# Kernel tuning notes

Hardware: AMD Instinct MI355X
Metric: run time of the kernel (lower is better)

Reference implementation:

```python
import jax, jax.numpy as jnp
import numpy as np

D_MODEL, D_K, D_V = 512, 64, 64
LN_EPS = 1e-6


def setup_inputs() -> dict:
    key = jax.random.key(0)
    ks = jax.random.split(key, 8)
    B, Lq, Lk = 2, 1024, 1024
    q = jax.random.normal(ks[0], (B, Lq, D_MODEL), dtype=jnp.float32)
    k = jax.random.normal(ks[1], (B, Lk, D_MODEL), dtype=jnp.float32)
    v = jax.random.normal(ks[2], (B, Lk, D_MODEL), dtype=jnp.float32)
    s = 1.0 / np.sqrt(D_MODEL)
    Wq = jax.random.normal(ks[3], (D_MODEL, D_K), dtype=jnp.float32) * s
    Wk = jax.random.normal(ks[4], (D_MODEL, D_K), dtype=jnp.float32) * s
    Wv = jax.random.normal(ks[5], (D_MODEL, D_V), dtype=jnp.float32) * s
    v_param = jax.random.normal(ks[6], (D_K,), dtype=jnp.float32)
    Wfc = jax.random.normal(ks[7], (D_V, D_MODEL), dtype=jnp.float32) / np.sqrt(D_V)
    ln_gamma = jnp.ones((D_MODEL,), dtype=jnp.float32)
    ln_beta = jnp.zeros((D_MODEL,), dtype=jnp.float32)
    return {"q": q, "k": k, "v": v, "Wq": Wq, "Wk": Wk, "Wv": Wv,
            "v_param": v_param, "Wfc": Wfc, "ln_gamma": ln_gamma, "ln_beta": ln_beta}


def reference(q, k, v, Wq, Wk, Wv, v_param, Wfc, ln_gamma, ln_beta):
    residual = q
    qp = q @ Wq                      # [B, Lq, d_k]
    kp = k @ Wk                      # [B, Lk, d_k]
    vp = v @ Wv                      # [B, Lk, d_v]
    # additive (Bahdanau) scores: tanh(q_i + k_j) . v_param  -> [B, Lq, Lk]
    scores = jnp.einsum("bqkd,d->bqk", jnp.tanh(qp[:, :, None, :] + kp[:, None, :, :]), v_param)
    attn = jax.nn.softmax(scores, axis=-1)   # dropout is identity in eval mode
    out = jnp.einsum("bqk,bkv->bqv", attn, vp)
    out = out @ Wfc + residual               # [B, Lq, d_model]
    mu = jnp.mean(out, axis=-1, keepdims=True)
    var = jnp.var(out, axis=-1, keepdims=True)
    out = (out - mu) * jax.lax.rsqrt(var + LN_EPS) * ln_gamma + ln_beta
    return out, attn
```

## Files before the change

kernel.cpp:

```cpp
#include <hip/hip_runtime.h>
#include <cstddef>
#include <cstdint>

#define D_MODEL 512
#define DK 64
#define LQ 1024
#define LK 1024
#define NB 2
#define LN_EPS 1e-6f
#define L2E2 2.8853900817779268f

__device__ __forceinline__ uint32_t pack_bf2(float a, float b) {
  uint32_t ua = __float_as_uint(a), ub = __float_as_uint(b);
  ua = (ua + 0x7fffu + ((ua >> 16) & 1u)) >> 16;
  ub = (ub + 0x7fffu + ((ub >> 16) & 1u)) >> 16;
  return (ub << 16) | ua;
}

#define PR_ROWS 32
__global__ __launch_bounds__(512) void proj_kernel(
    const float* __restrict__ q, const float* __restrict__ k,
    const float* __restrict__ v, const float* __restrict__ Wq,
    const float* __restrict__ Wk, const float* __restrict__ Wv,
    const float* __restrict__ v_param, float2* __restrict__ ab_g,
    uint32_t* __restrict__ ekT, float* __restrict__ vp) {
  __shared__ float rows[PR_ROWS][D_MODEL];
  const int tid = threadIdx.x;
  const int type = blockIdx.x >> 6;
  const int r0 = (blockIdx.x & 63) * PR_ROWS;
  const float* __restrict__ in = (type == 0) ? q : (type == 1) ? k : v;
  const float* __restrict__ W = (type == 0) ? Wq : (type == 1) ? Wk : Wv;
  {
    const float4* __restrict__ in4 = (const float4*)(in + (size_t)r0 * D_MODEL);
    float4* r4 = (float4*)&rows[0][0];
#pragma unroll
    for (int t = 0; t < 8; ++t) r4[tid + 512 * t] = in4[tid + 512 * t];
  }
  __syncthreads();
  const int lane = tid & 63;
  const int wv = tid >> 6;
  const int rglob = r0 + wv * 4;
  const float* __restrict__ Wl = W + lane;
  float c0[4] = {0.f, 0.f, 0.f, 0.f}, c1[4] = {0.f, 0.f, 0.f, 0.f};
#pragma unroll 2
  for (int e = 0; e < D_MODEL; e += 4) {
    float w0 = Wl[(size_t)(e + 0) * DK];
    float w1 = Wl[(size_t)(e + 1) * DK];
    float w2 = Wl[(size_t)(e + 2) * DK];
    float w3 = Wl[(size_t)(e + 3) * DK];
#pragma unroll
    for (int r = 0; r < 4; ++r) {
      float4 x = *(const float4*)&rows[wv * 4 + r][e];
      c0[r] = fmaf(x.x, w0, c0[r]);
      c1[r] = fmaf(x.y, w1, c1[r]);
      c0[r] = fmaf(x.z, w2, c0[r]);
      c1[r] = fmaf(x.w, w3, c1[r]);
    }
  }
  float acc[4];
#pragma unroll
  for (int r = 0; r < 4; ++r) acc[r] = c0[r] + c1[r];
  if (type == 0) {
    float vpar = v_param[lane];
#pragma unroll
    for (int r = 0; r < 4; ++r) {
      float iv = __builtin_amdgcn_exp2f(-L2E2 * acc[r]);
      ab_g[(size_t)(rglob + r) * DK + lane] = make_float2(vpar * iv, iv);
    }
  } else if (type == 1) {
    float e4[4], h4[4];
#pragma unroll
    for (int r = 0; r < 4; ++r) {
      e4[r] = __builtin_amdgcn_exp2f(L2E2 * acc[r]);
      h4[r] = __shfl_down(e4[r], 32);
    }
    if (lane < 32) {
      int b = rglob >> 10, j0 = rglob & 1023;
      uint4 pk;
      pk.x = pack_bf2(e4[0], h4[0]);
      pk.y = pack_bf2(e4[1], h4[1]);
      pk.z = pack_bf2(e4[2], h4[2]);
      pk.w = pack_bf2(e4[3], h4[3]);
      *(uint4*)&ekT[(size_t)b * 32 * LK + (size_t)lane * LK + j0] = pk;
    }
  } else {
#pragma unroll
    for (int r = 0; r < 4; ++r)
      vp[(size_t)(rglob + r) * DK + lane] = acc[r];
  }
}

#define RB 8
__global__ __launch_bounds__(1024, 4) void attn_kernel(
    const float2* __restrict__ ab_g, const uint32_t* __restrict__ ekT,
    const float* __restrict__ vp, const float* __restrict__ resid,
    const float* __restrict__ Wfc, const float* __restrict__ gamma,
    const float* __restrict__ beta, float* __restrict__ out,
    float* __restrict__ attn_out) {
  __shared__ float sc[RB][LK];
  __shared__ float4 ab4s[RB][32];
  __shared__ float4 pvred[16][RB][16];
  __shared__ __align__(16) float ovlT[DK][RB];
  __shared__ float mred[RB][2], sred[RB][2];
  __shared__ float red[2][RB][8];
  const int tid = threadIdx.x;
  const int row0 = blockIdx.x * RB;
  const int batch = row0 >> 10;
  const uint32_t* __restrict__ ekT_b = ekT + (size_t)batch * 32 * LK;
  const float* __restrict__ vp_b = vp + (size_t)batch * LK * DK;

  if (tid < RB * 64) {
    int r = tid >> 6, d = tid & 63;
    float2 abv = ab_g[(size_t)(row0 + r) * DK + d];
    ((float2*)&ab4s[r][d & 31])[d >> 5] = abv;
  }
  __syncthreads();

  {
    const int j = tid;
    float acc[RB];
#pragma unroll
    for (int r = 0; r < RB; ++r) acc[r] = 0.f;
#pragma unroll 4
    for (int dp = 0; dp < 32; ++dp) {
      uint32_t kw = ekT_b[(size_t)dp * LK + j];
      float klo = __uint_as_float(kw << 16);
      float khi = __uint_as_float(kw & 0xffff0000u);
#pragma unroll
      for (int r = 0; r < RB; ++r) {
        float4 ab = ab4s[r][dp];
        float x1 = klo + ab.y, x2 = khi + ab.w;
        float num = fmaf(ab.z, x1, ab.x * x2);
        acc[r] = fmaf(num, __builtin_amdgcn_rcpf(x1 * x2), acc[r]);
      }
    }
#pragma unroll
    for (int r = 0; r < RB; ++r) sc[r][j] = acc[r];
  }
  __syncthreads();

  const int wave = __builtin_amdgcn_readfirstlane(tid >> 6);
  const int lane = tid & 63;

  {
    const int row = wave >> 1, half = wave & 1;
    const int jb = half * 512;
    float m = 1e30f;
#pragma unroll
    for (int i = 0; i < 8; ++i) m = fminf(m, sc[row][jb + i * 64 + lane]);
#pragma unroll
    for (int off = 32; off > 0; off >>= 1) m = fminf(m, __shfl_xor(m, off));
    if (lane == 0) mred[row][half] = m;
    __syncthreads();
    m = fminf(mred[row][0], mred[row][1]);
    float p[8];
    float ssum = 0.f;
#pragma unroll
    for (int i = 0; i < 8; ++i) {
      float e = __builtin_amdgcn_exp2f((m - sc[row][jb + i * 64 + lane]) * L2E2);
      p[i] = e;
      ssum += e;
    }
#pragma unroll
    for (int off = 32; off > 0; off >>= 1) ssum += __shfl_xor(ssum, off);
    if (lane == 0) sred[row][half] = ssum;
    __syncthreads();
    float inv = __builtin_amdgcn_rcpf(sred[row][0] + sred[row][1]);
    float* __restrict__ arow = attn_out + (size_t)(row0 + row) * LK;
#pragma unroll
    for (int i = 0; i < 8; ++i) {
      float pn = p[i] * inv;
      sc[row][jb + i * 64 + lane] = pn;
      arow[jb + i * 64 + lane] = pn;
    }
  }
  __syncthreads();

  {
    const int jj = lane >> 4, l16 = lane & 15;
    const float4* __restrict__ vp4 = (const float4*)vp_b;
    float4 a[RB];
#pragma unroll
    for (int r = 0; r < RB; ++r) a[r] = make_float4(0.f, 0.f, 0.f, 0.f);
#pragma unroll 2
    for (int it = 0; it < 16; ++it) {
      int j = (wave << 6) + (it << 2) + jj;
      float4 vv = vp4[(size_t)j * (DK / 4) + l16];
#pragma unroll
      for (int r = 0; r < RB; ++r) {
        float pw = sc[r][j];
        a[r].x = fmaf(pw, vv.x, a[r].x);
        a[r].y = fmaf(pw, vv.y, a[r].y);
        a[r].z = fmaf(pw, vv.z, a[r].z);
        a[r].w = fmaf(pw, vv.w, a[r].w);
      }
    }
#pragma unroll
    for (int r = 0; r < RB; ++r) {
      a[r].x += __shfl_xor(a[r].x, 16); a[r].y += __shfl_xor(a[r].y, 16);
      a[r].z += __shfl_xor(a[r].z, 16); a[r].w += __shfl_xor(a[r].w, 16);
      a[r].x += __shfl_xor(a[r].x, 32); a[r].y += __shfl_xor(a[r].y, 32);
      a[r].z += __shfl_xor(a[r].z, 32); a[r].w += __shfl_xor(a[r].w, 32);
    }
    if (jj == 0) {
#pragma unroll
      for (int r = 0; r < RB; ++r) pvred[wave][r][l16] = a[r];
    }
  }
  __syncthreads();
  if (tid < 128) {
    int r = tid >> 4, l16 = tid & 15;
    float4 s = make_float4(0.f, 0.f, 0.f, 0.f);
#pragma unroll
    for (int w = 0; w < 16; ++w) {
      float4 t = pvred[w][r][l16];
      s.x += t.x; s.y += t.y; s.z += t.z; s.w += t.w;
    }
    ovlT[l16 * 4 + 0][r] = s.x;
    ovlT[l16 * 4 + 1][r] = s.y;
    ovlT[l16 * 4 + 2][r] = s.z;
    ovlT[l16 * 4 + 3][r] = s.w;
  }
  __syncthreads();

  {
    const int g = tid >> 9, c = tid & 511, rbase = g * 4;
    const int wv8 = (tid >> 6) & 7;
    float y[4];
#pragma unroll
    for (int rr = 0; rr < 4; ++rr)
      y[rr] = resid[(size_t)(row0 + rbase + rr) * D_MODEL + c];
#pragma unroll 4
    for (int e = 0; e < DK; ++e) {
      float w = Wfc[(size_t)e * D_MODEL + c];
      float4 ov = *(const float4*)&ovlT[e][rbase];
      y[0] = fmaf(ov.x, w, y[0]);
      y[1] = fmaf(ov.y, w, y[1]);
      y[2] = fmaf(ov.z, w, y[2]);
      y[3] = fmaf(ov.w, w, y[3]);
    }
#pragma unroll
    for (int rr = 0; rr < 4; ++rr) {
      float s = y[rr];
#pragma unroll
      for (int off = 32; off > 0; off >>= 1) s += __shfl_xor(s, off);
      if (lane == 0) red[0][rbase + rr][wv8] = s;
    }
    __syncthreads();
    float mu[4];
#pragma unroll
    for (int rr = 0; rr < 4; ++rr) {
      float s = 0.f;
#pragma unroll
      for (int w = 0; w < 8; ++w) s += red[0][rbase + rr][w];
      mu[rr] = s * (1.0f / D_MODEL);
    }
#pragma unroll
    for (int rr = 0; rr < 4; ++rr) {
      float d = y[rr] - mu[rr];
      float s = d * d;
#pragma unroll
      for (int off = 32; off > 0; off >>= 1) s += __shfl_xor(s, off);
      if (lane == 0) red[1][rbase + rr][wv8] = s;
    }
    __syncthreads();
    float gg = gamma[c], bb = beta[c];
#pragma unroll
    for (int rr = 0; rr < 4; ++rr) {
      float s = 0.f;
#pragma unroll
      for (int w = 0; w < 8; ++w) s += red[1][rbase + rr][w];
      float var = s * (1.0f / D_MODEL);
      float rstd = rsqrtf(var + LN_EPS);
      out[(size_t)(row0 + rbase + rr) * D_MODEL + c] =
          (y[rr] - mu[rr]) * rstd * gg + bb;
    }
  }
}

extern "C" void kernel_launch(void* const* d_in, const int* in_sizes, int n_in,
                              void* d_out, int out_size, void* d_ws,
                              size_t ws_size, hipStream_t stream) {
  const float* q = (const float*)d_in[0];
  const float* k = (const float*)d_in[1];
  const float* v = (const float*)d_in[2];
  const float* Wq = (const float*)d_in[3];
  const float* Wk = (const float*)d_in[4];
  const float* Wv = (const float*)d_in[5];
  const float* v_param = (const float*)d_in[6];
  const float* Wfc = (const float*)d_in[7];
  const float* gamma = (const float*)d_in[8];
  const float* beta = (const float*)d_in[9];

  float* out = (float*)d_out;
  float* attn = out + (size_t)NB * LQ * D_MODEL;

  float* base = (float*)d_ws;
  float2* ab_g = (float2*)base;
  uint32_t* ekT = (uint32_t*)(base + (size_t)2 * NB * LQ * DK);
  float* vp = base + (size_t)2 * NB * LQ * DK + NB * 32 * LK;

  hipLaunchKernelGGL(proj_kernel, dim3(3 * 64), dim3(512), 0, stream, q, k, v,
                     Wq, Wk, Wv, v_param, ab_g, ekT, vp);
  hipLaunchKernelGGL(attn_kernel, dim3(NB * LQ / RB), dim3(1024), 0, stream,
                     ab_g, ekT, vp, q, Wfc, gamma, beta, out, attn);
}
```

Measured before the change: 64.92 us.

## Split attention kernel into score/softmax and PV+FC+LayerNorm kernels with smaller blocks

Splits the fused 1024-thread attention kernel into two 256-thread kernels. The first computes scores and softmax in registers, four rows by four columns per thread, and writes attn. The second reloads attn from global memory to do the PV product, the FC projection and LayerNorm. The projection kernel also drops to 16 rows per 256-thread block, doubling its grid. The goal is higher occupancy and better latency hiding through smaller blocks. The cost is an extra launch and an extra global round trip of the attention matrix.

```diff
diff --git a/kernel.cpp b/kernel.cpp
--- a/kernel.cpp
+++ b/kernel.cpp
@@ -17,8 +17,8 @@
   return (ub << 16) | ua;
 }
 
-#define PR_ROWS 32
-__global__ __launch_bounds__(512) void proj_kernel(
+#define PR_ROWS 16
+__global__ __launch_bounds__(256, 4) void proj_kernel(
     const float* __restrict__ q, const float* __restrict__ k,
     const float* __restrict__ v, const float* __restrict__ Wq,
     const float* __restrict__ Wk, const float* __restrict__ Wv,
@@ -26,15 +26,15 @@
     uint32_t* __restrict__ ekT, float* __restrict__ vp) {
   __shared__ float rows[PR_ROWS][D_MODEL];
   const int tid = threadIdx.x;
-  const int type = blockIdx.x >> 6;
-  const int r0 = (blockIdx.x & 63) * PR_ROWS;
+  const int type = blockIdx.x >> 7;
+  const int r0 = (blockIdx.x & 127) * PR_ROWS;
   const float* __restrict__ in = (type == 0) ? q : (type == 1) ? k : v;
   const float* __restrict__ W = (type == 0) ? Wq : (type == 1) ? Wk : Wv;
   {
     const float4* __restrict__ in4 = (const float4*)(in + (size_t)r0 * D_MODEL);
     float4* r4 = (float4*)&rows[0][0];
 #pragma unroll
-    for (int t = 0; t < 8; ++t) r4[tid + 512 * t] = in4[tid + 512 * t];
+    for (int t = 0; t < 8; ++t) r4[tid + 256 * t] = in4[tid + 256 * t];
   }
   __syncthreads();
   const int lane = tid & 63;
@@ -85,96 +85,121 @@
     }
   } else {
 #pragma unroll
-    for (int r = 0; r < 4; ++r)
-      vp[(size_t)(rglob + r) * DK + lane] = acc[r];
-  }
-}
-
-#define RB 8
-__global__ __launch_bounds__(1024, 4) void attn_kernel(
+    for (int r = 0; r < 4; ++r) vp[(size_t)(rglob + r) * DK + lane] = acc[r];
+  }
+}
+
+#define RB 4
+__global__ __launch_bounds__(256, 6) void score_kernel(
     const float2* __restrict__ ab_g, const uint32_t* __restrict__ ekT,
-    const float* __restrict__ vp, const float* __restrict__ resid,
-    const float* __restrict__ Wfc, const float* __restrict__ gamma,
-    const float* __restrict__ beta, float* __restrict__ out,
     float* __restrict__ attn_out) {
-  __shared__ float sc[RB][LK];
   __shared__ float4 ab4s[RB][32];
-  __shared__ float4 pvred[16][RB][16];
-  __shared__ __align__(16) float ovlT[DK][RB];
-  __shared__ float mred[RB][2], sred[RB][2];
-  __shared__ float red[2][RB][8];
+  __shared__ float mred[RB][4], sred[RB][4];
   const int tid = threadIdx.x;
   const int row0 = blockIdx.x * RB;
   const int batch = row0 >> 10;
   const uint32_t* __restrict__ ekT_b = ekT + (size_t)batch * 32 * LK;
-  const float* __restrict__ vp_b = vp + (size_t)batch * LK * DK;
-
-  if (tid < RB * 64) {
+  {
     int r = tid >> 6, d = tid & 63;
     float2 abv = ab_g[(size_t)(row0 + r) * DK + d];
     ((float2*)&ab4s[r][d & 31])[d >> 5] = abv;
   }
   __syncthreads();
 
-  {
-    const int j = tid;
-    float acc[RB];
-#pragma unroll
-    for (int r = 0; r < RB; ++r) acc[r] = 0.f;
-#pragma unroll 4
-    for (int dp = 0; dp < 32; ++dp) {
-      uint32_t kw = ekT_b[(size_t)dp * LK + j];
-      float klo = __uint_as_float(kw << 16);
-      float khi = __uint_as_float(kw & 0xffff0000u);
-#pragma unroll
-      for (int r = 0; r < RB; ++r) {
-        float4 ab = ab4s[r][dp];
-        float x1 = klo + ab.y, x2 = khi + ab.w;
+  float acc[RB][4];
+#pragma unroll
+  for (int r = 0; r < RB; ++r)
+#pragma unroll
+    for (int jj = 0; jj < 4; ++jj) acc[r][jj] = 0.f;
+
+#pragma unroll 2
+  for (int dp = 0; dp < 32; ++dp) {
+    float klo[4], khi[4];
+#pragma unroll
+    for (int jj = 0; jj < 4; ++jj) {
+      uint32_t kw = ekT_b[(size_t)dp * LK + tid + jj * 256];
+      klo[jj] = __uint_as_float(kw << 16);
+      khi[jj] = __uint_as_float(kw & 0xffff0000u);
+    }
+#pragma unroll
+    for (int r = 0; r < RB; ++r) {
+      float4 ab = ab4s[r][dp];
+#pragma unroll
+      for (int jj = 0; jj < 4; ++jj) {
+        float x1 = klo[jj] + ab.y, x2 = khi[jj] + ab.w;
         float num = fmaf(ab.z, x1, ab.x * x2);
-        acc[r] = fmaf(num, __builtin_amdgcn_rcpf(x1 * x2), acc[r]);
+        acc[r][jj] = fmaf(num, __builtin_amdgcn_rcpf(x1 * x2), acc[r][jj]);
       }
     }
-#pragma unroll
-    for (int r = 0; r < RB; ++r) sc[r][j] = acc[r];
-  }
-  __syncthreads();
+  }
 
   const int wave = __builtin_amdgcn_readfirstlane(tid >> 6);
   const int lane = tid & 63;
 
   {
-    const int row = wave >> 1, half = wave & 1;
-    const int jb = half * 512;
-    float m = 1e30f;
-#pragma unroll
-    for (int i = 0; i < 8; ++i) m = fminf(m, sc[row][jb + i * 64 + lane]);
-#pragma unroll
-    for (int off = 32; off > 0; off >>= 1) m = fminf(m, __shfl_xor(m, off));
-    if (lane == 0) mred[row][half] = m;
+#pragma unroll
+    for (int r = 0; r < RB; ++r) {
+      float pm = fminf(fminf(acc[r][0], acc[r][1]), fminf(acc[r][2], acc[r][3]));
+#pragma unroll
+      for (int off = 32; off > 0; off >>= 1) pm = fminf(pm, __shfl_xor(pm, off));
+      if (lane == 0) mred[r][wave] = pm;
+    }
     __syncthreads();
-    m = fminf(mred[row][0], mred[row][1]);
-    float p[8];
-    float ssum = 0.f;
-#pragma unroll
-    for (int i = 0; i < 8; ++i) {
-      float e = __builtin_amdgcn_exp2f((m - sc[row][jb + i * 64 + lane]) * L2E2);
-      p[i] = e;
-      ssum += e;
-    }
-#pragma unroll
-    for (int off = 32; off > 0; off >>= 1) ssum += __shfl_xor(ssum, off);
-    if (lane == 0) sred[row][half] = ssum;
+    float inv[RB];
+#pragma unroll
+    for (int r = 0; r < RB; ++r) {
+      float m = fminf(fminf(mred[r][0], mred[r][1]),
+                      fminf(mred[r][2], mred[r][3]));
+      float s = 0.f;
+#pragma unroll
+      for (int jj = 0; jj < 4; ++jj) {
+        float e = __builtin_amdgcn_exp2f((m - acc[r][jj]) * L2E2);
+        acc[r][jj] = e;
+        s += e;
+      }
+#pragma unroll
+      for (int off = 32; off > 0; off >>= 1) s += __shfl_xor(s, off);
+      if (lane == 0) sred[r][wave] = s;
+    }
     __syncthreads();
-    float inv = __builtin_amdgcn_rcpf(sred[row][0] + sred[row][1]);
-    float* __restrict__ arow = attn_out + (size_t)(row0 + row) * LK;
-#pragma unroll
-    for (int i = 0; i < 8; ++i) {
-      float pn = p[i] * inv;
-      sc[row][jb + i * 64 + lane] = pn;
-      arow[jb + i * 64 + lane] = pn;
-    }
-  }
-  __syncthreads();
+#pragma unroll
+    for (int r = 0; r < RB; ++r)
+      inv[r] = __builtin_amdgcn_rcpf(sred[r][0] + sred[r][1] + sred[r][2] +
+                                     sred[r][3]);
+#pragma unroll
+    for (int r = 0; r < RB; ++r) {
+      float* __restrict__ arow = attn_out + (size_t)(row0 + r) * LK;
+#pragma unroll
+      for (int jj = 0; jj < 4; ++jj)
+        arow[tid + jj * 256] = acc[r][jj] * inv[r];
+    }
+  }
+}
+
+__global__ __launch_bounds__(256, 4) void pvfc_kernel(
+    const float* __restrict__ attn, const float* __restrict__ vp,
+    const float* __restrict__ resid, const float* __restrict__ Wfc,
+    const float* __restrict__ gamma, const float* __restrict__ beta,
+    float* __restrict__ out) {
+  __shared__ float sc[RB][LK];
+  __shared__ float4 pvred[4][RB][16];
+  __shared__ __align__(16) float ovlT[DK][RB];
+  __shared__ float red[2][RB][4];
+  const int tid = threadIdx.x;
+  const int row0 = blockIdx.x * RB;
+  const int batch = row0 >> 10;
+  const float* __restrict__ vp_b = vp + (size_t)batch * LK * DK;
+  {
+    const float4* __restrict__ a4 =
+        (const float4*)(attn + (size_t)row0 * LK);
+    float4* s4 = (float4*)&sc[0][0];
+#pragma unroll
+    for (int t = 0; t < 4; ++t) s4[tid + 256 * t] = a4[tid + 256 * t];
+  }
+  __syncthreads();
+
+  const int wave = __builtin_amdgcn_readfirstlane(tid >> 6);
+  const int lane = tid & 63;
 
   {
     const int jj = lane >> 4, l16 = lane & 15;
@@ -182,9 +207,9 @@
     float4 a[RB];
 #pragma unroll
     for (int r = 0; r < RB; ++r) a[r] = make_float4(0.f, 0.f, 0.f, 0.f);
-#pragma unroll 2
-    for (int it = 0; it < 16; ++it) {
-      int j = (wave << 6) + (it << 2) + jj;
+#pragma unroll 4
+    for (int it = 0; it < 64; ++it) {
+      int j = (wave << 8) + (it << 2) + jj;
       float4 vv = vp4[(size_t)j * (DK / 4) + l16];
 #pragma unroll
       for (int r = 0; r < RB; ++r) {
@@ -208,11 +233,11 @@
     }
   }
   __syncthreads();
-  if (tid < 128) {
+  if (tid < 64) {
     int r = tid >> 4, l16 = tid & 15;
     float4 s = make_float4(0.f, 0.f, 0.f, 0.f);
 #pragma unroll
-    for (int w = 0; w < 16; ++w) {
+    for (int w = 0; w < 4; ++w) {
       float4 t = pvred[w][r][l16];
       s.x += t.x; s.y += t.y; s.z += t.z; s.w += t.w;
     }
@@ -224,56 +249,53 @@
   __syncthreads();
 
   {
-    const int g = tid >> 9, c = tid & 511, rbase = g * 4;
-    const int wv8 = (tid >> 6) & 7;
-    float y[4];
-#pragma unroll
-    for (int rr = 0; rr < 4; ++rr)
-      y[rr] = resid[(size_t)(row0 + rbase + rr) * D_MODEL + c];
+    const int c0 = tid, c1 = tid + 256;
+    float y[RB][2];
+#pragma unroll
+    for (int r = 0; r < RB; ++r) {
+      y[r][0] = resid[(size_t)(row0 + r) * D_MODEL + c0];
+      y[r][1] = resid[(size_t)(row0 + r) * D_MODEL + c1];
+    }
 #pragma unroll 4
     for (int e = 0; e < DK; ++e) {
-      float w = Wfc[(size_t)e * D_MODEL + c];
-      float4 ov = *(const float4*)&ovlT[e][rbase];
-      y[0] = fmaf(ov.x, w, y[0]);
-      y[1] = fmaf(ov.y, w, y[1]);
-      y[2] = fmaf(ov.z, w, y[2]);
-      y[3] = fmaf(ov.w, w, y[3]);
-    }
-#pragma unroll
-    for (int rr = 0; rr < 4; ++rr) {
-      float s = y[rr];
+      float w0 = Wfc[(size_t)e * D_MODEL + c0];
+      float w1 = Wfc[(size_t)e * D_MODEL + c1];
+      float4 ov = *(const float4*)&ovlT[e][0];
+      y[0][0] = fmaf(ov.x, w0, y[0][0]); y[0][1] = fmaf(ov.x, w1, y[0][1]);
+      y[1][0] = fmaf(ov.y, w0, y[1][0]); y[1][1] = fmaf(ov.y, w1, y[1][1]);
+      y[2][0] = fmaf(ov.z, w0, y[2][0]); y[2][1] = fmaf(ov.z, w1, y[2][1]);
+      y[3][0] = fmaf(ov.w, w0, y[3][0]); y[3][1] = fmaf(ov.w, w1, y[3][1]);
+    }
+#pragma unroll
+    for (int r = 0; r < RB; ++r) {
+      float s = y[r][0] + y[r][1];
 #pragma unroll
       for (int off = 32; off > 0; off >>= 1) s += __shfl_xor(s, off);
-      if (lane == 0) red[0][rbase + rr][wv8] = s;
+      if (lane == 0) red[0][r][wave] = s;
     }
     __syncthreads();
-    float mu[4];
-#pragma unroll
-    for (int rr = 0; rr < 4; ++rr) {
-      float s = 0.f;
-#pragma unroll
-      for (int w = 0; w < 8; ++w) s += red[0][rbase + rr][w];
-      mu[rr] = s * (1.0f / D_MODEL);
-    }
-#pragma unroll
-    for (int rr = 0; rr < 4; ++rr) {
-      float d = y[rr] - mu[rr];
-      float s = d * d;
+    float mu[RB];
+#pragma unroll
+    for (int r = 0; r < RB; ++r)
+      mu[r] = (red[0][r][0] + red[0][r][1] + red[0][r][2] + red[0][r][3]) *
+              (1.0f / D_MODEL);
+#pragma unroll
+    for (int r = 0; r < RB; ++r) {
+      float d0 = y[r][0] - mu[r], d1 = y[r][1] - mu[r];
+      float s = d0 * d0 + d1 * d1;
 #pragma unroll
       for (int off = 32; off > 0; off >>= 1) s += __shfl_xor(s, off);
-      if (lane == 0) red[1][rbase + rr][wv8] = s;
+      if (lane == 0) red[1][r][wave] = s;
     }
     __syncthreads();
-    float gg = gamma[c], bb = beta[c];
-#pragma unroll
-    for (int rr = 0; rr < 4; ++rr) {
-      float s = 0.f;
-#pragma unroll
-      for (int w = 0; w < 8; ++w) s += red[1][rbase + rr][w];
-      float var = s * (1.0f / D_MODEL);
+    float g0 = gamma[c0], g1 = gamma[c1], b0 = beta[c0], b1 = beta[c1];
+#pragma unroll
+    for (int r = 0; r < RB; ++r) {
+      float var = (red[1][r][0] + red[1][r][1] + red[1][r][2] + red[1][r][3]) *
+                  (1.0f / D_MODEL);
       float rstd = rsqrtf(var + LN_EPS);
-      out[(size_t)(row0 + rbase + rr) * D_MODEL + c] =
-          (y[rr] - mu[rr]) * rstd * gg + bb;
+      out[(size_t)(row0 + r) * D_MODEL + c0] = (y[r][0] - mu[r]) * rstd * g0 + b0;
+      out[(size_t)(row0 + r) * D_MODEL + c1] = (y[r][1] - mu[r]) * rstd * g1 + b1;
     }
   }
 }
@@ -300,8 +322,10 @@
   uint32_t* ekT = (uint32_t*)(base + (size_t)2 * NB * LQ * DK);
   float* vp = base + (size_t)2 * NB * LQ * DK + NB * 32 * LK;
 
-  hipLaunchKernelGGL(proj_kernel, dim3(3 * 64), dim3(512), 0, stream, q, k, v,
+  hipLaunchKernelGGL(proj_kernel, dim3(3 * 128), dim3(256), 0, stream, q, k, v,
                      Wq, Wk, Wv, v_param, ab_g, ekT, vp);
-  hipLaunchKernelGGL(attn_kernel, dim3(NB * LQ / RB), dim3(1024), 0, stream,
-                     ab_g, ekT, vp, q, Wfc, gamma, beta, out, attn);
-}
+  hipLaunchKernelGGL(score_kernel, dim3(NB * LQ / RB), dim3(256), 0, stream,
+                     ab_g, ekT, attn);
+  hipLaunchKernelGGL(pvfc_kernel, dim3(NB * LQ / RB), dim3(256), 0, stream,
+                     attn, vp, q, Wfc, gamma, beta, out);
+}
```

New measurement: 63.92 us. About the same (-1.5%).
